# Performance work log

Hardware: AMD Instinct MI355X
Metric: run time of the kernel (lower is better)

The kernel has to match this reference:

```python
import jax, jax.numpy as jnp
import numpy as np

BIGNET_DIM = 1024
GROUP = 16
N_LIN = 15  # 6 blocks (last has no LN after) x 3 QLoRALinear
N_LN = 5
LORA_SCALE = 0.125  # 1/8
LN_EPS = 1e-5


def setup_inputs() -> dict:
    key = jax.random.key(0)
    ks = jax.random.split(key, 8)
    B = 8192
    x = jax.random.normal(ks[0], (B, BIGNET_DIM), dtype=jnp.float32)
    # 4-bit codes in [0, 16), group-wise fp16 scales (absmax-like, positive)
    q_w = jax.random.randint(ks[1], (N_LIN, BIGNET_DIM, BIGNET_DIM), 0, 16, dtype=jnp.int32)
    scales = (jax.random.uniform(ks[2], (N_LIN, BIGNET_DIM, BIGNET_DIM // GROUP)) * 0.05 + 0.01).astype(jnp.float16)
    biases = (jax.random.normal(ks[3], (N_LIN, BIGNET_DIM)) * 0.01).astype(jnp.float16)
    lora_A = jax.random.normal(ks[4], (N_LIN, 32, BIGNET_DIM), dtype=jnp.float32) * (1.0 / np.sqrt(BIGNET_DIM))
    # lora_B is zero-init in the module; use small random values so the LoRA path is exercised
    lora_B = jax.random.normal(ks[5], (N_LIN, BIGNET_DIM, 32), dtype=jnp.float32) * 0.01
    ln_g = jnp.ones((N_LN, BIGNET_DIM), dtype=jnp.float32)
    ln_b = jnp.zeros((N_LN, BIGNET_DIM), dtype=jnp.float32)
    return {"x": x, "q_w": q_w, "scales": scales, "biases": biases,
            "lora_A": lora_A, "lora_B": lora_B, "ln_g": ln_g, "ln_b": ln_b}


def _dequant4bit(q, scale):
    # q: [out, in] int codes in [0,16); scale: [out, in//GROUP] fp16
    # w = (q / 15 * 2 - 1) * group_scale, computed in fp16 like the torch code
    s = jnp.repeat(scale, GROUP, axis=1)  # [out, in]
    return (q.astype(jnp.float16) * jnp.float16(2.0 / 15.0) - jnp.float16(1.0)) * s


def _qlora_linear(x, q, scale, bias, A, B):
    w = _dequant4bit(q, scale)                                   # [out, in] f16
    half = jnp.dot(x.astype(jnp.float16), w.T) + bias            # f16 GEMM
    lora = jnp.dot(jnp.dot(x, A.T), B.T) * LORA_SCALE            # f32 rank-32 path
    return half.astype(jnp.float32) + lora


def _layernorm(x, g, b):
    mu = jnp.mean(x, axis=-1, keepdims=True)
    var = jnp.mean(jnp.square(x - mu), axis=-1, keepdims=True)
    return (x - mu) * jax.lax.rsqrt(var + LN_EPS) * g + b


def _forward(x, q_w, scales, biases, lora_A, lora_B, ln_g, ln_b):
    h = x
    li = 0
    for blk in range(6):
        r = h
        for j in range(3):
            r = _qlora_linear(r, q_w[li], scales[li], biases[li], lora_A[li], lora_B[li])
            li += 1
            if j < 2:
                r = jax.nn.relu(r)
        h = r + h  # block residual
        if blk < 5:
            h = _layernorm(h, ln_g[blk], ln_b[blk])
    return h


def reference(x, q_w, scales, biases, lora_A, lora_B, ln_g, ln_b):
    return _forward(x, q_w, scales, biases, lora_A, lora_B, ln_g, ln_b)
```

## Files before the change

### kernel.cpp

```cpp
#include <hip/hip_runtime.h>

typedef _Float16 f16;
typedef _Float16 f16x8 __attribute__((ext_vector_type(8)));
typedef _Float16 f16x4 __attribute__((ext_vector_type(4)));
typedef float f32x4 __attribute__((ext_vector_type(4)));

__global__ void detect_kernel(const unsigned short* __restrict__ sc, int* __restrict__ mode)
{
    if (threadIdx.x != 0 || blockIdx.x != 0) return;
    bool ok16 = true, okbf = true;
    for (int i = 0; i < 64; i++) {
        const unsigned short b = sc[i];
        union { unsigned short u; f16 h; } ch; ch.u = b;
        const float fv = (float)ch.h;
        if (!(fv > 0.008f && fv < 0.062f)) ok16 = false;
        union { unsigned int u; float f; } cb; cb.u = ((unsigned int)b) << 16;
        if (!(cb.f > 0.008f && cb.f < 0.062f)) okbf = false;
    }
    *mode = ok16 ? 0 : (okbf ? 1 : 2);
}

__device__ __forceinline__ float load_half_like(const void* p, int i, int mode)
{
    if (mode == 0) return (float)((const f16*)p)[i];
    if (mode == 1) {
        union { unsigned int u; float f; } c;
        c.u = ((unsigned int)((const unsigned short*)p)[i]) << 16;
        return c.f;
    }
    return ((const float*)p)[i];
}

__global__ void prep_kernel(const float* __restrict__ x, const int* __restrict__ qw,
                            const void* __restrict__ scales, const void* __restrict__ biases,
                            const float* __restrict__ lA, const float* __restrict__ lB,
                            const int* __restrict__ modep,
                            f16* __restrict__ Wdq, f16* __restrict__ A16,
                            f16* __restrict__ B16, f16* __restrict__ x16,
                            float* __restrict__ bias32)
{
    const int bid = blockIdx.x, tid = threadIdx.x;
    if (bid < 3840) {
        const int md = *modep;
        const int g = bid * 256 + tid;
        const float s = load_half_like(scales, g, md);
        const int4* qp = (const int4*)(qw + (size_t)g * 16);
        f16x8 w0, w1;
        #pragma unroll
        for (int v = 0; v < 4; v++) {
            const int4 q4 = qp[v];
            const int qs[4] = {q4.x, q4.y, q4.z, q4.w};
            #pragma unroll
            for (int j = 0; j < 4; j++) {
                f16 t = (f16)qs[j];
                t = t * (f16)(2.0f / 15.0f);
                t = t - (f16)1.0f;
                const f16 w = (f16)((float)t * s);
                if (v < 2) w0[v * 4 + j] = w; else w1[(v - 2) * 4 + j] = w;
            }
        }
        *(f16x8*)(Wdq + (size_t)g * 16) = w0;
        *(f16x8*)(Wdq + (size_t)g * 16 + 8) = w1;
    } else if (bid < 4320) {
        const int i = (bid - 3840) * 1024 + tid * 4;
        const float4 a = *(const float4*)(lA + i);
        f16x4 o = {(f16)a.x, (f16)a.y, (f16)a.z, (f16)a.w};
        *(f16x4*)(A16 + i) = o;
    } else if (bid < 4800) {
        const int i = (bid - 4320) * 1024 + tid * 4;
        const float4 a = *(const float4*)(lB + i);
        f16x4 o = {(f16)(0.125f * a.x), (f16)(0.125f * a.y),
                   (f16)(0.125f * a.z), (f16)(0.125f * a.w)};
        *(f16x4*)(B16 + i) = o;
    } else if (bid < 12992) {
        const int i = (bid - 4800) * 1024 + tid * 4;
        const float4 a = *(const float4*)(x + i);
        f16x4 o = {(f16)a.x, (f16)a.y, (f16)a.z, (f16)a.w};
        *(f16x4*)(x16 + i) = o;
    } else {
        const int md = *modep;
        const int i = (bid - 12992) * 1024 + tid * 4;
        float4 o;
        o.x = load_half_like(biases, i, md);
        o.y = load_half_like(biases, i + 1, md);
        o.z = load_half_like(biases, i + 2, md);
        o.w = load_half_like(biases, i + 3, md);
        *(float4*)(bias32 + i) = o;
    }
}

__global__ __launch_bounds__(256, 2)
void layer_kernel(const f16* __restrict__ X16, const f16* __restrict__ W,
                  const f16* __restrict__ AL, const f16* __restrict__ BL,
                  const float* __restrict__ biasL, const float* __restrict__ resid,
                  float* __restrict__ out32, f16* __restrict__ out16, int do_relu)
{
    __shared__ __align__(16) f16 lds[36864];

    const int tid  = threadIdx.x;
    const int lane = tid & 63;
    const int wv   = tid >> 6;
    const int wy   = wv >> 1, wx = wv & 1;
    const int by   = blockIdx.x & 63;
    const int bx   = blockIdx.x >> 6;
    const int row0 = by << 7;
    const int col0 = bx << 7;

    const int lr = lane >> 3;
    const int pc = lane & 7;
    const int gk = pc << 3;
    const int wc = ((pc ^ lr) << 3);

    const int m15 = lane & 15;
    const int q2  = lane >> 4;
    const int sw  = m15 & 7;
    const int po0 = ((q2 ^ sw) << 3);
    const int po1 = (((4 + q2) ^ sw) << 3);
    const int q8  = q2 << 3;

    f32x4 acc[4][4] = {};
    f32x4 tacc[2][2] = {};
    f16x8 rx[2][4], rw[2][4], rl[2];

    auto gload = [&](int kt, int slot) {
        const int kb = kt << 6;
        #pragma unroll
        for (int i = 0; i < 4; i++) {
            rx[slot][i] = *(const f16x8*)(X16 + (size_t)(row0 + wv * 32 + i * 8 + lr) * 1024 + kb + gk);
            rw[slot][i] = *(const f16x8*)(W   + (size_t)(col0 + wv * 32 + i * 8 + lr) * 1024 + kb + gk);
        }
        rl[slot] = *(const f16x8*)(AL + (size_t)(wv * 8 + lr) * 1024 + kb + gk);
    };
    auto swrite = [&](f16* buf, int slot) {
        #pragma unroll
        for (int i = 0; i < 4; i++) {
            *(f16x8*)(buf + (wv * 32 + i * 8 + lr) * 64 + wc) = rx[slot][i];
            *(f16x8*)(buf + 8192 + (wv * 32 + i * 8 + lr) * 64 + wc) = rw[slot][i];
        }
        *(f16x8*)(buf + 16384 + (wv * 8 + lr) * 64 + wc) = rl[slot];
    };

    gload(0, 0);
    gload(1, 1);
    swrite(lds, 0);

    for (int kt = 0; kt < 16; kt++) {
        __syncthreads();
        const f16* cur = lds + (kt & 1) * 18432;
        const f16* sA = cur;
        const f16* sB = cur + 8192;
        const f16* sL = cur + 16384;

        f16x8 af[2][4], bf[2][4], lf[2][2];
        #pragma unroll
        for (int s = 0; s < 2; s++) {
            const int po = s ? po1 : po0;
            #pragma unroll
            for (int mi = 0; mi < 4; mi++)
                af[s][mi] = *(const f16x8*)(sA + (wy * 64 + mi * 16 + m15) * 64 + po);
            #pragma unroll
            for (int ni = 0; ni < 4; ni++)
                bf[s][ni] = *(const f16x8*)(sB + (wx * 64 + ni * 16 + m15) * 64 + po);
            #pragma unroll
            for (int pi = 0; pi < 2; pi++)
                lf[s][pi] = *(const f16x8*)(sL + (pi * 16 + m15) * 64 + po);
        }

        if (kt < 14) gload(kt + 2, kt & 1);

        #pragma unroll
        for (int s = 0; s < 2; s++) {
            #pragma unroll
            for (int mi = 0; mi < 4; mi++)
                #pragma unroll
                for (int ni = 0; ni < 4; ni++)
                    acc[mi][ni] = __builtin_amdgcn_mfma_f32_16x16x32_f16(af[s][mi], bf[s][ni], acc[mi][ni], 0, 0, 0);
            #pragma unroll
            for (int mi = 0; mi < 2; mi++)
                #pragma unroll
                for (int pi = 0; pi < 2; pi++)
                    tacc[mi][pi] = __builtin_amdgcn_mfma_f32_16x16x32_f16(af[s][2 * wx + mi], lf[s][pi], tacc[mi][pi], 0, 0, 0);
        }

        __builtin_amdgcn_sched_barrier(0);
        if (kt < 15) swrite(lds + ((kt + 1) & 1) * 18432, (kt + 1) & 1);
    }

    __syncthreads();
    float* Tl = (float*)lds;
    const int q4 = (lane >> 4) << 2;
    {
        #pragma unroll
        for (int mi = 0; mi < 2; mi++)
            #pragma unroll
            for (int pi = 0; pi < 2; pi++)
                #pragma unroll
                for (int r = 0; r < 4; r++)
                    Tl[(wy * 64 + wx * 32 + mi * 16 + q4 + r) * 33 + pi * 16 + m15] = tacc[mi][pi][r];
    }
    __syncthreads();

    f16x8 tf[4];
    #pragma unroll
    for (int mi = 0; mi < 4; mi++) {
        const float* tp = Tl + (wy * 64 + mi * 16 + m15) * 33 + q8;
        f16x8 v;
        #pragma unroll
        for (int j = 0; j < 8; j++) v[j] = (f16)tp[j];
        tf[mi] = v;
    }
    f16x8 bfr[4]; float bb[4];
    #pragma unroll
    for (int ni = 0; ni < 4; ni++) {
        const int colg = col0 + wx * 64 + ni * 16 + m15;
        bfr[ni] = *(const f16x8*)(BL + (size_t)colg * 32 + q8);
        bb[ni] = biasL[colg];
    }
    #pragma unroll
    for (int mi = 0; mi < 4; mi++)
        #pragma unroll
        for (int ni = 0; ni < 4; ni++) {
            #pragma unroll
            for (int r = 0; r < 4; r++)
                acc[mi][ni][r] += bb[ni];
            acc[mi][ni] = __builtin_amdgcn_mfma_f32_16x16x32_f16(tf[mi], bfr[ni], acc[mi][ni], 0, 0, 0);
        }

    __syncthreads();
    if (out16) {
        f16* ot = lds;
        #pragma unroll
        for (int mi = 0; mi < 4; mi++)
            #pragma unroll
            for (int ni = 0; ni < 4; ni++)
                #pragma unroll
                for (int r = 0; r < 4; r++) {
                    float v = acc[mi][ni][r];
                    if (do_relu) v = fmaxf(v, 0.0f);
                    ot[(wy * 64 + mi * 16 + q4 + r) * 136 + wx * 64 + ni * 16 + m15] = (f16)v;
                }
        __syncthreads();
        const int rr = tid >> 4;
        const int cc = (tid & 15) << 3;
        #pragma unroll
        for (int it = 0; it < 8; it++) {
            const int r = it * 16 + rr;
            const f16x8 v = *(const f16x8*)(ot + r * 136 + cc);
            *(f16x8*)(out16 + (size_t)(row0 + r) * 1024 + col0 + cc) = v;
        }
    } else {
        float* otf = (float*)lds;
        const int rr = tid >> 5;
        const int cc = (tid & 31) << 2;
        #pragma unroll
        for (int half = 0; half < 2; half++) {
            if (wy == half) {
                #pragma unroll
                for (int mi = 0; mi < 4; mi++)
                    #pragma unroll
                    for (int ni = 0; ni < 4; ni++)
                        #pragma unroll
                        for (int r = 0; r < 4; r++)
                            otf[(mi * 16 + q4 + r) * 140 + wx * 64 + ni * 16 + m15] = acc[mi][ni][r];
            }
            __syncthreads();
            #pragma unroll
            for (int it = 0; it < 8; it++) {
                const int r = it * 8 + rr;
                f32x4 v = *(const f32x4*)(otf + r * 140 + cc);
                const size_t gidx = (size_t)(row0 + half * 64 + r) * 1024 + col0 + cc;
                const f32x4 rs = *(const f32x4*)(resid + gidx);
                v += rs;
                *(f32x4*)(out32 + gidx) = v;
            }
            if (half == 0) __syncthreads();
        }
    }
}

__global__ void ln_kernel(float* __restrict__ h, f16* __restrict__ h16,
                          const float* __restrict__ g, const float* __restrict__ b)
{
    const int row = blockIdx.x, tid = threadIdx.x;
    float* hp = h + (size_t)row * 1024;
    const int c = tid * 4;
    const float4 v = *(const float4*)(hp + c);
    float s = v.x + v.y + v.z + v.w;
    #pragma unroll
    for (int off = 32; off > 0; off >>= 1) s += __shfl_down(s, off);
    __shared__ float r1[4], r2[4];
    const int wv = tid >> 6, lane = tid & 63;
    if (lane == 0) r1[wv] = s;
    __syncthreads();
    const float mu = (r1[0] + r1[1] + r1[2] + r1[3]) * (1.0f / 1024.0f);
    const float dx = v.x - mu, dy = v.y - mu, dz = v.z - mu, dw = v.w - mu;
    float s2 = dx * dx + dy * dy + dz * dz + dw * dw;
    #pragma unroll
    for (int off = 32; off > 0; off >>= 1) s2 += __shfl_down(s2, off);
    if (lane == 0) r2[wv] = s2;
    __syncthreads();
    const float var = (r2[0] + r2[1] + r2[2] + r2[3]) * (1.0f / 1024.0f);
    const float rs = 1.0f / sqrtf(var + 1e-5f);
    float4 o;
    o.x = dx * rs * g[c]     + b[c];
    o.y = dy * rs * g[c + 1] + b[c + 1];
    o.z = dz * rs * g[c + 2] + b[c + 2];
    o.w = dw * rs * g[c + 3] + b[c + 3];
    *(float4*)(hp + c) = o;
    f16x4 o16 = {(f16)o.x, (f16)o.y, (f16)o.z, (f16)o.w};
    *(f16x4*)(h16 + (size_t)row * 1024 + c) = o16;
}

extern "C" void kernel_launch(void* const* d_in, const int* in_sizes, int n_in,
                              void* d_out, int out_size, void* d_ws, size_t ws_size,
                              hipStream_t stream)
{
    const float* x      = (const float*)d_in[0];
    const int*   qw     = (const int*)d_in[1];
    const void*  scales = d_in[2];
    const void*  biases = d_in[3];
    const float* lA     = (const float*)d_in[4];
    const float* lB     = (const float*)d_in[5];
    const float* lng    = (const float*)d_in[6];
    const float* lnb    = (const float*)d_in[7];
    float* out = (float*)d_out;

    char* ws = (char*)d_ws;
    int*   mode   = (int*)(ws);
    float* bias32 = (float*)(ws + 64);
    f16* Wdq = (f16*)(ws + 65536u);
    f16* A16 = (f16*)(ws + 31522816u);
    f16* B16 = (f16*)(ws + 32505856u);
    f16* fA  = (f16*)(ws + 33488896u);
    f16* fB  = (f16*)(ws + 50266112u);
    float* h32 = out;

    detect_kernel<<<1, 64, 0, stream>>>((const unsigned short*)scales, mode);
    prep_kernel<<<13007, 256, 0, stream>>>(x, qw, scales, biases, lA, lB, mode,
                                           Wdq, A16, B16, fA, bias32);

    int li = 0;
    for (int blk = 0; blk < 6; blk++) {
        const float* resid = (blk == 0) ? x : h32;
        for (int j = 0; j < 3; j++, li++) {
            const int wl = li < 15 ? li : 14;
            const f16* in16 = (j == 1) ? fB : fA;
            f16* o16 = (j == 0) ? fB : (j == 1 ? fA : (f16*)nullptr);
            float* o32 = nullptr;
            const float* rz = nullptr;
            if (j == 2) { o32 = h32; rz = resid; }
            layer_kernel<<<512, 256, 0, stream>>>(in16,
                Wdq + (size_t)wl * 1048576,
                A16 + (size_t)wl * 32768,
                B16 + (size_t)wl * 32768,
                bias32 + (size_t)wl * 1024,
                rz, o32, o16, j < 2 ? 1 : 0);
        }
        if (blk < 5)
            ln_kernel<<<8192, 256, 0, stream>>>(h32, fA, lng + blk * 1024, lnb + blk * 1024);
    }
}
```

Measured before the change: 1.367 ms.

## Stage GEMM tiles directly from global memory into LDS with global_load_lds

Replaces the register-staged prefetch (global load into VGPRs, then an LDS store) with direct global-to-LDS loads via the global_load_lds builtin. The XOR swizzle now goes on the global-side column offset, so each lane's linear LDS slot matches the old swizzled layout. The next tile is issued right after the barrier into the other buffer. This removes the staging registers and the explicit LDS write instructions, which frees VGPRs and issue slots, but cuts prefetch depth from two tiles to one. It also relies on the load completing before the next barrier.

```diff
diff --git a/kernel.cpp b/kernel.cpp
--- a/kernel.cpp
+++ b/kernel.cpp
@@ -89,6 +89,13 @@
     }
 }
 
+__device__ __forceinline__ void gl_lds16(const f16* g, f16* l)
+{
+    __builtin_amdgcn_global_load_lds(
+        (const __attribute__((address_space(1))) void*)g,
+        (__attribute__((address_space(3))) void*)l, 16, 0, 0);
+}
+
 __global__ __launch_bounds__(256, 2)
 void layer_kernel(const f16* __restrict__ X16, const f16* __restrict__ W,
                   const f16* __restrict__ AL, const f16* __restrict__ BL,
@@ -108,8 +115,7 @@
 
     const int lr = lane >> 3;
     const int pc = lane & 7;
-    const int gk = pc << 3;
-    const int wc = ((pc ^ lr) << 3);
+    const int gksw = ((pc ^ lr) << 3);
 
     const int m15 = lane & 15;
     const int q2  = lane >> 4;
@@ -120,29 +126,21 @@
 
     f32x4 acc[4][4] = {};
     f32x4 tacc[2][2] = {};
-    f16x8 rx[2][4], rw[2][4], rl[2];
-
-    auto gload = [&](int kt, int slot) {
-        const int kb = kt << 6;
+
+    auto stage = [&](f16* buf, int kt) {
+        const int kb = (kt << 6) + gksw;
         #pragma unroll
         for (int i = 0; i < 4; i++) {
-            rx[slot][i] = *(const f16x8*)(X16 + (size_t)(row0 + wv * 32 + i * 8 + lr) * 1024 + kb + gk);
-            rw[slot][i] = *(const f16x8*)(W   + (size_t)(col0 + wv * 32 + i * 8 + lr) * 1024 + kb + gk);
-        }
-        rl[slot] = *(const f16x8*)(AL + (size_t)(wv * 8 + lr) * 1024 + kb + gk);
+            gl_lds16(X16 + (size_t)(row0 + wv * 32 + i * 8 + lr) * 1024 + kb,
+                     buf + (wv * 32 + i * 8) * 64);
+            gl_lds16(W + (size_t)(col0 + wv * 32 + i * 8 + lr) * 1024 + kb,
+                     buf + 8192 + (wv * 32 + i * 8) * 64);
+        }
+        gl_lds16(AL + (size_t)(wv * 8 + lr) * 1024 + kb,
+                 buf + 16384 + wv * 8 * 64);
     };
-    auto swrite = [&](f16* buf, int slot) {
-        #pragma unroll
-        for (int i = 0; i < 4; i++) {
-            *(f16x8*)(buf + (wv * 32 + i * 8 + lr) * 64 + wc) = rx[slot][i];
-            *(f16x8*)(buf + 8192 + (wv * 32 + i * 8 + lr) * 64 + wc) = rw[slot][i];
-        }
-        *(f16x8*)(buf + 16384 + (wv * 8 + lr) * 64 + wc) = rl[slot];
-    };
-
-    gload(0, 0);
-    gload(1, 1);
-    swrite(lds, 0);
+
+    stage(lds, 0);
 
     for (int kt = 0; kt < 16; kt++) {
         __syncthreads();
@@ -151,6 +149,8 @@
         const f16* sB = cur + 8192;
         const f16* sL = cur + 16384;
 
+        if (kt < 15) stage(lds + ((kt + 1) & 1) * 18432, kt + 1);
+
         f16x8 af[2][4], bf[2][4], lf[2][2];
         #pragma unroll
         for (int s = 0; s < 2; s++) {
@@ -166,8 +166,6 @@
                 lf[s][pi] = *(const f16x8*)(sL + (pi * 16 + m15) * 64 + po);
         }
 
-        if (kt < 14) gload(kt + 2, kt & 1);
-
         #pragma unroll
         for (int s = 0; s < 2; s++) {
             #pragma unroll
@@ -181,9 +179,6 @@
                 for (int pi = 0; pi < 2; pi++)
                     tacc[mi][pi] = __builtin_amdgcn_mfma_f32_16x16x32_f16(af[s][2 * wx + mi], lf[s][pi], tacc[mi][pi], 0, 0, 0);
         }
-
-        __builtin_amdgcn_sched_barrier(0);
-        if (kt < 15) swrite(lds + ((kt + 1) & 1) * 18432, (kt + 1) & 1);
     }
 
     __syncthreads();
```

After: 1.380 ms. Within noise of the previous version (+1.0%).

## Restructure GEMM main loop with named register buffers and explicit waitcnt pipelining

Applied to the files above, without the earlier changes.

Replaces the slot-indexed prefetch register arrays with two named register sets and unrolls the k-loop by two, so the buffer selection is resolved at compile time instead of by dynamic indexing. Explicit s_waitcnt vmcnt/lgkmcnt waits and a single s_barrier after each LDS write replace the loop-top __syncthreads. LDS fragment reads are now split per k-substep to lower register pressure, and the next global prefetch is issued between those reads and the MFMAs. The hand-placed waits depend on exact load counts, and an unused, oddly written lambda is left in the code.

```diff
diff --git a/kernel.cpp b/kernel.cpp
--- a/kernel.cpp
+++ b/kernel.cpp
@@ -120,70 +120,127 @@
 
     f32x4 acc[4][4] = {};
     f32x4 tacc[2][2] = {};
-    f16x8 rx[2][4], rw[2][4], rl[2];
-
-    auto gload = [&](int kt, int slot) {
-        const int kb = kt << 6;
+
+    f16x8 ax0[4], aw0[4], al0;
+    f16x8 ax1[4], aw1[4], al1;
+
+    auto gload = [&](int kt, f16x8 (&sx)[4], f16x8 (&swr)[4], f16x8 &sl) {
+        const int kb = (kt << 6) + gk;
         #pragma unroll
         for (int i = 0; i < 4; i++) {
-            rx[slot][i] = *(const f16x8*)(X16 + (size_t)(row0 + wv * 32 + i * 8 + lr) * 1024 + kb + gk);
-            rw[slot][i] = *(const f16x8*)(W   + (size_t)(col0 + wv * 32 + i * 8 + lr) * 1024 + kb + gk);
-        }
-        rl[slot] = *(const f16x8*)(AL + (size_t)(wv * 8 + lr) * 1024 + kb + gk);
+            sx[i]  = *(const f16x8*)(X16 + (size_t)(row0 + wv * 32 + i * 8 + lr) * 1024 + kb);
+            swr[i] = *(const f16x8*)(W   + (size_t)(col0 + wv * 32 + i * 8 + lr) * 1024 + kb);
+        }
+        sl = *(const f16x8*)(AL + (size_t)(wv * 8 + lr) * 1024 + kb);
     };
-    auto swrite = [&](f16* buf, int slot) {
+    auto swrite = [&](int bsel, f16x8 (&sx)[4], f16x8 (&swr)[4], f16x8 &sl) {
+        f16* buf = lds + bsel * 18432;
         #pragma unroll
         for (int i = 0; i < 4; i++) {
-            *(f16x8*)(buf + (wv * 32 + i * 8 + lr) * 64 + wc) = rx[slot][i];
-            *(f16x8*)(buf + 8192 + (wv * 32 + i * 8 + lr) * 64 + wc) = rw[slot][i];
-        }
-        *(f16x8*)(buf + 16384 + (wv * 8 + lr) * 64 + wc) = rl[slot];
+            *(f16x8*)(buf + (wv * 32 + i * 8 + lr) * 64 + wc) = sx[i];
+            *(f16x8*)(buf + 8192 + (wv * 32 + i * 8 + lr) * 64 + wc) = swr[i];
+        }
+        *(f16x8*)(buf + 16384 + (wv * 8 + lr) * 64 + wc) = sl;
     };
 
-    gload(0, 0);
-    gload(1, 1);
-    swrite(lds, 0);
-
-    for (int kt = 0; kt < 16; kt++) {
-        __syncthreads();
+    gload(0, ax0, aw0, al0);
+    gload(1, ax1, aw1, al1);
+    asm volatile("s_waitcnt vmcnt(9)" ::: "memory");
+    __builtin_amdgcn_sched_barrier(0);
+    swrite(0, ax0, aw0, al0);
+    asm volatile("s_waitcnt lgkmcnt(0)" ::: "memory");
+    __builtin_amdgcn_s_barrier();
+
+    auto step = [&](int kt, f16x8 (&rx)[4], f16x8 (&rw)[4], f16x8 &rl,
+                            f16x8 (&px)[4], f16x8 (&pw)[4], f16x8 &pl) {
         const f16* cur = lds + (kt & 1) * 18432;
         const f16* sA = cur;
         const f16* sB = cur + 8192;
         const f16* sL = cur + 16384;
 
-        f16x8 af[2][4], bf[2][4], lf[2][2];
         #pragma unroll
         for (int s = 0; s < 2; s++) {
             const int po = s ? po1 : po0;
+            f16x8 af[4], bf[4], lf[2];
             #pragma unroll
             for (int mi = 0; mi < 4; mi++)
-                af[s][mi] = *(const f16x8*)(sA + (wy * 64 + mi * 16 + m15) * 64 + po);
+                af[mi] = *(const f16x8*)(sA + (wy * 64 + mi * 16 + m15) * 64 + po);
             #pragma unroll
             for (int ni = 0; ni < 4; ni++)
-                bf[s][ni] = *(const f16x8*)(sB + (wx * 64 + ni * 16 + m15) * 64 + po);
+                bf[ni] = *(const f16x8*)(sB + (wx * 64 + ni * 16 + m15) * 64 + po);
             #pragma unroll
             for (int pi = 0; pi < 2; pi++)
-                lf[s][pi] = *(const f16x8*)(sL + (pi * 16 + m15) * 64 + po);
-        }
-
-        if (kt < 14) gload(kt + 2, kt & 1);
-
-        #pragma unroll
-        for (int s = 0; s < 2; s++) {
+                lf[pi] = *(const f16x8*)(sL + (pi * 16 + m15) * 64 + po);
+            if (s == 0 && kt < 14) gload(kt + 2, rx, rw, rl);
+            asm volatile("s_waitcnt lgkmcnt(0)" ::: "memory");
+            __builtin_amdgcn_sched_barrier(0);
             #pragma unroll
             for (int mi = 0; mi < 4; mi++)
                 #pragma unroll
                 for (int ni = 0; ni < 4; ni++)
-                    acc[mi][ni] = __builtin_amdgcn_mfma_f32_16x16x32_f16(af[s][mi], bf[s][ni], acc[mi][ni], 0, 0, 0);
+                    acc[mi][ni] = __builtin_amdgcn_mfma_f32_16x16x32_f16(af[mi], bf[ni], acc[mi][ni], 0, 0, 0);
             #pragma unroll
             for (int mi = 0; mi < 2; mi++)
                 #pragma unroll
                 for (int pi = 0; pi < 2; pi++)
-                    tacc[mi][pi] = __builtin_amdgcn_mfma_f32_16x16x32_f16(af[s][2 * wx + mi], lf[s][pi], tacc[mi][pi], 0, 0, 0);
-        }
-
-        __builtin_amdgcn_sched_barrier(0);
-        if (kt < 15) swrite(lds + ((kt + 1) & 1) * 18432, (kt + 1) & 1);
+                    tacc[mi][pi] = __builtin_amdgcn_mfma_f32_16x16x32_f16(af[s ? 2 : 2 * wx + mi - mi, 0] , lf[pi], tacc[mi][pi], 0, 0, 0);
+        }
+    };
+    (void)step;
+
+    {
+        #pragma unroll 1
+        for (int k2 = 0; k2 < 8; k2++) {
+            #pragma unroll
+            for (int half = 0; half < 2; half++) {
+                const int kt = 2 * k2 + half;
+                const f16* cur = lds + (kt & 1) * 18432;
+                const f16* sA = cur;
+                const f16* sB = cur + 8192;
+                const f16* sL = cur + 16384;
+
+                #pragma unroll
+                for (int s = 0; s < 2; s++) {
+                    const int po = s ? po1 : po0;
+                    f16x8 af[4], bf[4], lf[2];
+                    #pragma unroll
+                    for (int mi = 0; mi < 4; mi++)
+                        af[mi] = *(const f16x8*)(sA + (wy * 64 + mi * 16 + m15) * 64 + po);
+                    #pragma unroll
+                    for (int ni = 0; ni < 4; ni++)
+                        bf[ni] = *(const f16x8*)(sB + (wx * 64 + ni * 16 + m15) * 64 + po);
+                    #pragma unroll
+                    for (int pi = 0; pi < 2; pi++)
+                        lf[pi] = *(const f16x8*)(sL + (pi * 16 + m15) * 64 + po);
+                    if (s == 0 && kt < 14) {
+                        if (half == 0) gload(kt + 2, ax0, aw0, al0);
+                        else           gload(kt + 2, ax1, aw1, al1);
+                    }
+                    asm volatile("s_waitcnt lgkmcnt(0)" ::: "memory");
+                    __builtin_amdgcn_sched_barrier(0);
+                    #pragma unroll
+                    for (int mi = 0; mi < 4; mi++)
+                        #pragma unroll
+                        for (int ni = 0; ni < 4; ni++)
+                            acc[mi][ni] = __builtin_amdgcn_mfma_f32_16x16x32_f16(af[mi], bf[ni], acc[mi][ni], 0, 0, 0);
+                    #pragma unroll
+                    for (int mi = 0; mi < 2; mi++)
+                        #pragma unroll
+                        for (int pi = 0; pi < 2; pi++)
+                            tacc[mi][pi] = __builtin_amdgcn_mfma_f32_16x16x32_f16(af[2 * wx + mi], lf[pi], tacc[mi][pi], 0, 0, 0);
+                }
+
+                if (kt < 15) {
+                    if (kt < 14) asm volatile("s_waitcnt vmcnt(9)" ::: "memory");
+                    else         asm volatile("s_waitcnt vmcnt(0)" ::: "memory");
+                    __builtin_amdgcn_sched_barrier(0);
+                    if (half == 0) swrite((kt + 1) & 1, ax1, aw1, al1);
+                    else           swrite((kt + 1) & 1, ax0, aw0, al0);
+                    asm volatile("s_waitcnt lgkmcnt(0)" ::: "memory");
+                    __builtin_amdgcn_s_barrier();
+                }
+            }
+        }
     }
 
     __syncthreads();
```

After: 1.449 ms. +6.0%, slower.
